# Kernel tuning notes

Measured on AMD Instinct MI355X. Metric: run time of the kernel, lower is better.

## Reference

```python
import jax, jax.numpy as jnp
import numpy as np


def setup_inputs() -> dict:
    key = jax.random.key(0)
    kq, kk, kv = jax.random.split(key, 3)
    n, d = 8192, 32
    return {
        "Q": jax.random.normal(kq, (n, d), dtype=jnp.float32),
        "K": jax.random.normal(kk, (n, d), dtype=jnp.float32),
        "V": jax.random.normal(kv, (n, d), dtype=jnp.float32),
    }


def reference(Q, K, V):
    # FlashAttention-2 tiling with online softmax is mathematically equivalent
    # to full (unscaled, unmasked) softmax attention: O = softmax(Q K^T) V.
    # Note: the original module applies NO 1/sqrt(d) scaling.
    S = jnp.einsum("qd,kd->qk", Q, K)           # [n, n]
    P = jax.nn.softmax(S, axis=-1)                # numerically stable softmax
    return jnp.einsum("qk,kd->qd", P, V)         # [n, d]
```

## Files before the change

### kernel.cpp

```cpp
#include <hip/hip_runtime.h>
#include <hip/hip_bf16.h>

typedef __bf16 bf16x8 __attribute__((ext_vector_type(8)));
typedef __bf16 bf16x4 __attribute__((ext_vector_type(4)));
typedef float  f32x4  __attribute__((ext_vector_type(4)));
typedef unsigned short u16;

static constexpr int N = 8192;
static constexpr int D = 32;
static constexpr float L2E = 1.44269504088896340736f;
static constexpr float MSHIFT = 32.0f;

__device__ __forceinline__ void gl_lds16(const u16* g, u16* l) {
  __builtin_amdgcn_global_load_lds(
      (const __attribute__((address_space(1))) unsigned int*)g,
      (__attribute__((address_space(3))) unsigned int*)l, 16, 0, 0);
}

__global__ __launch_bounds__(256) void prep_kernel(
    const float* __restrict__ Q, const float* __restrict__ K,
    const float* __restrict__ V, u16* __restrict__ Qb, u16* __restrict__ Kb,
    u16* __restrict__ Vt) {
  __shared__ float tile[64][33];
  const int b = blockIdx.x;
  auto pack = [](float x, float y) -> unsigned int {
    u16 ux = __builtin_bit_cast(u16, (__bf16)x);
    u16 uy = __builtin_bit_cast(u16, (__bf16)y);
    return (unsigned int)ux | ((unsigned int)uy << 16);
  };
  if (b < 256) {
    const int i = (b * 256 + threadIdx.x) * 4;
    const float4 q = *reinterpret_cast<const float4*>(Q + i);
    const float4 k = *reinterpret_cast<const float4*>(K + i);
    uint2 qo = { pack(q.x * L2E, q.y * L2E), pack(q.z * L2E, q.w * L2E) };
    uint2 ko = { pack(k.x, k.y), pack(k.z, k.w) };
    *reinterpret_cast<uint2*>(Qb + i) = qo;
    *reinterpret_cast<uint2*>(Kb + i) = ko;
  } else {
    const int r0 = (b - 256) * 64;
    const int row = threadIdx.x >> 2;
    const int c0 = (threadIdx.x & 3) * 8;
    const float4 x0 = *reinterpret_cast<const float4*>(V + (size_t)(r0 + row) * D + c0);
    const float4 x1 = *reinterpret_cast<const float4*>(V + (size_t)(r0 + row) * D + c0 + 4);
    tile[row][c0 + 0] = x0.x; tile[row][c0 + 1] = x0.y;
    tile[row][c0 + 2] = x0.z; tile[row][c0 + 3] = x0.w;
    tile[row][c0 + 4] = x1.x; tile[row][c0 + 5] = x1.y;
    tile[row][c0 + 6] = x1.z; tile[row][c0 + 7] = x1.w;
    __syncthreads();
    const int d = threadIdx.x >> 3;
    const int kc = (threadIdx.x & 7) * 8;
    uint4 o;
    o.x = pack(tile[kc + 0][d], tile[kc + 1][d]);
    o.y = pack(tile[kc + 2][d], tile[kc + 3][d]);
    o.z = pack(tile[kc + 4][d], tile[kc + 5][d]);
    o.w = pack(tile[kc + 6][d], tile[kc + 7][d]);
    *reinterpret_cast<uint4*>(Vt + (size_t)d * N + r0 + kc) = o;
  }
}

template <int NS>
__global__ __launch_bounds__(256, 4) void flash_kernel(
    const u16* __restrict__ Qb, const u16* __restrict__ Kb,
    const u16* __restrict__ Vt, float* __restrict__ lP,
    float* __restrict__ OP) {
  constexpr int KPB = N / NS;
  constexpr int NT = KPB / 64;
  __shared__ u16 Ks[2][2048];
  __shared__ u16 Vs[2][2048];

  const int tid = threadIdx.x;
  const int lane = tid & 63;
  const int wave = tid >> 6;
  const int a = lane & 15;
  const int g = lane >> 4;
  const int qg = blockIdx.x & 63;
  const int sp = blockIdx.x >> 6;
  const int qr0 = qg * 128 + wave * 32;
  const int k0 = sp * KPB;

  const bf16x8 qfA = *reinterpret_cast<const bf16x8*>(Qb + (qr0 + a) * D + g * 8);
  const bf16x8 qfB = *reinterpret_cast<const bf16x8*>(Qb + (qr0 + 16 + a) * D + g * 8);

  const int krow = tid >> 2;
  const int kslot = (tid & 3) ^ ((krow >> 1) & 3);
  const u16* __restrict__ ksrc = Kb + krow * D + kslot * 8;
  const int vd = tid >> 3;
  const int vlb = (tid & 7) ^ (vd & 7);
  const u16* __restrict__ vsrc = Vt + (size_t)vd * N + vlb * 8;
  u16* const kdst = &Ks[0][0] + wave * 512;
  u16* const vdst = &Vs[0][0] + wave * 512;

  const f32x4 minit = {-MSHIFT, -MSHIFT, -MSHIFT, -MSHIFT};
  const f32x4 zero4 = {0.f, 0.f, 0.f, 0.f};
  f32x4 accA0 = zero4, accA1 = zero4, accB0 = zero4, accB1 = zero4;
  float lA = 0.f, lB = 0.f;

  gl_lds16(ksrc + (size_t)k0 * D, kdst);
  gl_lds16(vsrc + k0, vdst);
  __syncthreads();

#pragma unroll
  for (int t = 0; t < NT; ++t) {
    const int cur = t & 1;
    if (t + 1 < NT) {
      const int kb = k0 + (t + 1) * 64;
      gl_lds16(ksrc + (size_t)kb * D, kdst + (cur ^ 1) * 2048);
      gl_lds16(vsrc + kb, vdst + (cur ^ 1) * 2048);
    }
    __builtin_amdgcn_sched_barrier(0);

    bf16x8 kf[4];
#pragma unroll
    for (int t4 = 0; t4 < 4; ++t4) {
      const int row = 16 * t4 + a;
      kf[t4] = *reinterpret_cast<const bf16x8*>(
          &Ks[cur][row * 32 + ((g ^ ((a >> 1) & 3)) << 3)]);
    }
    bf16x4 v0[4], v1[4];
#pragma unroll
    for (int tt = 0; tt < 4; ++tt) {
      const int pb = ((tt << 1) + (g >> 1)) ^ (a & 7);
      const int off = pb * 8 + (g & 1) * 4;
      v0[tt] = *reinterpret_cast<const bf16x4*>(&Vs[cur][a * 64 + off]);
      v1[tt] = *reinterpret_cast<const bf16x4*>(&Vs[cur][(16 + a) * 64 + off]);
    }

    f32x4 sA[4], sB[4];
#pragma unroll
    for (int t4 = 0; t4 < 4; ++t4) {
      sA[t4] = __builtin_amdgcn_mfma_f32_16x16x32_bf16(kf[t4], qfA, minit, 0, 0, 0);
      sB[t4] = __builtin_amdgcn_mfma_f32_16x16x32_bf16(kf[t4], qfB, minit, 0, 0, 0);
    }

    float pA[4][4], pB[4][4];
    float psA = 0.f, psB = 0.f;
#pragma unroll
    for (int t4 = 0; t4 < 4; ++t4) {
      float sa = 0.f, sb = 0.f;
#pragma unroll
      for (int r = 0; r < 4; ++r) {
        pA[t4][r] = __builtin_amdgcn_exp2f(sA[t4][r]);
        pB[t4][r] = __builtin_amdgcn_exp2f(sB[t4][r]);
        sa += pA[t4][r];
        sb += pB[t4][r];
      }
      psA += sa;
      psB += sb;
    }
    lA += psA;
    lB += psB;

    const bf16x8 pfA0 = {(__bf16)pA[0][0], (__bf16)pA[0][1], (__bf16)pA[0][2], (__bf16)pA[0][3],
                         (__bf16)pA[1][0], (__bf16)pA[1][1], (__bf16)pA[1][2], (__bf16)pA[1][3]};
    const bf16x8 pfA1 = {(__bf16)pA[2][0], (__bf16)pA[2][1], (__bf16)pA[2][2], (__bf16)pA[2][3],
                         (__bf16)pA[3][0], (__bf16)pA[3][1], (__bf16)pA[3][2], (__bf16)pA[3][3]};
    const bf16x8 pfB0 = {(__bf16)pB[0][0], (__bf16)pB[0][1], (__bf16)pB[0][2], (__bf16)pB[0][3],
                         (__bf16)pB[1][0], (__bf16)pB[1][1], (__bf16)pB[1][2], (__bf16)pB[1][3]};
    const bf16x8 pfB1 = {(__bf16)pB[2][0], (__bf16)pB[2][1], (__bf16)pB[2][2], (__bf16)pB[2][3],
                         (__bf16)pB[3][0], (__bf16)pB[3][1], (__bf16)pB[3][2], (__bf16)pB[3][3]};

    const bf16x8 va00 = __builtin_shufflevector(v0[0], v0[1], 0, 1, 2, 3, 4, 5, 6, 7);
    const bf16x8 va01 = __builtin_shufflevector(v0[2], v0[3], 0, 1, 2, 3, 4, 5, 6, 7);
    const bf16x8 va10 = __builtin_shufflevector(v1[0], v1[1], 0, 1, 2, 3, 4, 5, 6, 7);
    const bf16x8 va11 = __builtin_shufflevector(v1[2], v1[3], 0, 1, 2, 3, 4, 5, 6, 7);

    accA0 = __builtin_amdgcn_mfma_f32_16x16x32_bf16(va00, pfA0, accA0, 0, 0, 0);
    accA1 = __builtin_amdgcn_mfma_f32_16x16x32_bf16(va10, pfA0, accA1, 0, 0, 0);
    accB0 = __builtin_amdgcn_mfma_f32_16x16x32_bf16(va00, pfB0, accB0, 0, 0, 0);
    accB1 = __builtin_amdgcn_mfma_f32_16x16x32_bf16(va10, pfB0, accB1, 0, 0, 0);
    accA0 = __builtin_amdgcn_mfma_f32_16x16x32_bf16(va01, pfA1, accA0, 0, 0, 0);
    accA1 = __builtin_amdgcn_mfma_f32_16x16x32_bf16(va11, pfA1, accA1, 0, 0, 0);
    accB0 = __builtin_amdgcn_mfma_f32_16x16x32_bf16(va01, pfB1, accB0, 0, 0, 0);
    accB1 = __builtin_amdgcn_mfma_f32_16x16x32_bf16(va11, pfB1, accB1, 0, 0, 0);

    __syncthreads();
  }

  lA += __shfl_xor(lA, 16, 64);
  lA += __shfl_xor(lA, 32, 64);
  lB += __shfl_xor(lB, 16, 64);
  lB += __shfl_xor(lB, 32, 64);

  float* obA = OP + (size_t)(sp * N + qr0 + a) * D;
  float* obB = OP + (size_t)(sp * N + qr0 + 16 + a) * D;
#pragma unroll
  for (int r = 0; r < 4; ++r) {
    obA[4 * g + r] = accA0[r];
    obA[16 + 4 * g + r] = accA1[r];
    obB[4 * g + r] = accB0[r];
    obB[16 + 4 * g + r] = accB1[r];
  }
  if (g == 0) {
    lP[sp * N + qr0 + a] = lA;
    lP[sp * N + qr0 + 16 + a] = lB;
  }
}

template <int NS>
__global__ __launch_bounds__(256) void combine_kernel(
    const float* __restrict__ lP, const float* __restrict__ OP,
    float* __restrict__ out) {
  const int idx = blockIdx.x * 256 + threadIdx.x;
  if (idx >= N * D) return;
  const int q = idx >> 5;
  float L = 0.f, o = 0.f;
#pragma unroll
  for (int s = 0; s < NS; ++s) {
    L += lP[s * N + q];
    o += OP[(size_t)s * N * D + idx];
  }
  out[idx] = o / L;
}

extern "C" void kernel_launch(void* const* d_in, const int* in_sizes, int n_in,
                              void* d_out, int out_size, void* d_ws, size_t ws_size,
                              hipStream_t stream) {
  const float* Q = (const float*)d_in[0];
  const float* K = (const float*)d_in[1];
  const float* V = (const float*)d_in[2];
  float* out = (float*)d_out;

  const size_t base = (size_t)3 * N * D * sizeof(u16);
  const size_t per_split = (size_t)N * sizeof(float) + (size_t)N * D * sizeof(float);
  int ns = 16;
  while (ns > 4 && base + (size_t)ns * per_split > ws_size) ns >>= 1;

  u16* Qb = (u16*)d_ws;
  u16* Kb = Qb + N * D;
  u16* Vt = Kb + N * D;
  float* lP = (float*)(Vt + N * D);
  float* OP = lP + ns * N;

  prep_kernel<<<256 + N / 64, 256, 0, stream>>>(Q, K, V, Qb, Kb, Vt);
  switch (ns) {
    case 16:
      flash_kernel<16><<<64 * 16, 256, 0, stream>>>(Qb, Kb, Vt, lP, OP);
      combine_kernel<16><<<(N * D) / 256, 256, 0, stream>>>(lP, OP, out);
      break;
    case 8:
      flash_kernel<8><<<64 * 8, 256, 0, stream>>>(Qb, Kb, Vt, lP, OP);
      combine_kernel<8><<<(N * D) / 256, 256, 0, stream>>>(lP, OP, out);
      break;
    default:
      flash_kernel<4><<<64 * 4, 256, 0, stream>>>(Qb, Kb, Vt, lP, OP);
      combine_kernel<4><<<(N * D) / 256, 256, 0, stream>>>(lP, OP, out);
      break;
  }
}
```

Baseline: 33.91 us.

## Double key tile per iteration, add MFMA priority hints, vectorize partial-output stores and combine

The flash kernel now loads 128 keys per pipeline stage instead of 64, which halves the number of barriers and prefetch rounds. Each stage is processed as two 64-key halves with a new V swizzle for the 128-wide layout. It adds s_setprio around the MFMA groups and interleaves the A and B query halves so exp work can overlap with matrix ops. Partial-output stores and the combine kernel use float4 vectors, and the combine multiplies by a reciprocal instead of dividing. In exchange, LDS use doubles, which may reduce occupancy, and the fixed split count leaves fewer iterations to pipeline.

```diff
diff --git a/kernel.cpp b/kernel.cpp
--- a/kernel.cpp
+++ b/kernel.cpp
@@ -64,9 +64,9 @@
     const u16* __restrict__ Vt, float* __restrict__ lP,
     float* __restrict__ OP) {
   constexpr int KPB = N / NS;
-  constexpr int NT = KPB / 64;
-  __shared__ u16 Ks[2][2048];
-  __shared__ u16 Vs[2][2048];
+  constexpr int NT = KPB / 128;
+  __shared__ u16 Ks[2][4096];
+  __shared__ u16 Vs[2][4096];
 
   const int tid = threadIdx.x;
   const int lane = tid & 63;
@@ -84,9 +84,10 @@
   const int krow = tid >> 2;
   const int kslot = (tid & 3) ^ ((krow >> 1) & 3);
   const u16* __restrict__ ksrc = Kb + krow * D + kslot * 8;
-  const int vd = tid >> 3;
-  const int vlb = (tid & 7) ^ (vd & 7);
-  const u16* __restrict__ vsrc = Vt + (size_t)vd * N + vlb * 8;
+  const int vd = tid >> 4;
+  const int vblk = (tid & 15) ^ vd;
+  const u16* __restrict__ vsrcA = Vt + (size_t)vd * N + vblk * 8;
+  const u16* __restrict__ vsrcB = vsrcA + 16 * (size_t)N;
   u16* const kdst = &Ks[0][0] + wave * 512;
   u16* const vdst = &Vs[0][0] + wave * 512;
 
@@ -96,82 +97,114 @@
   float lA = 0.f, lB = 0.f;
 
   gl_lds16(ksrc + (size_t)k0 * D, kdst);
-  gl_lds16(vsrc + k0, vdst);
+  gl_lds16(ksrc + (size_t)(k0 + 64) * D, kdst + 2048);
+  gl_lds16(vsrcA + k0, vdst);
+  gl_lds16(vsrcB + k0, vdst + 2048);
   __syncthreads();
 
 #pragma unroll
   for (int t = 0; t < NT; ++t) {
     const int cur = t & 1;
     if (t + 1 < NT) {
-      const int kb = k0 + (t + 1) * 64;
-      gl_lds16(ksrc + (size_t)kb * D, kdst + (cur ^ 1) * 2048);
-      gl_lds16(vsrc + kb, vdst + (cur ^ 1) * 2048);
+      const int kb = k0 + (t + 1) * 128;
+      u16* kd = kdst + (cur ^ 1) * 4096;
+      u16* vd2 = vdst + (cur ^ 1) * 4096;
+      gl_lds16(ksrc + (size_t)kb * D, kd);
+      gl_lds16(ksrc + (size_t)(kb + 64) * D, kd + 2048);
+      gl_lds16(vsrcA + kb, vd2);
+      gl_lds16(vsrcB + kb, vd2 + 2048);
     }
     __builtin_amdgcn_sched_barrier(0);
 
-    bf16x8 kf[4];
-#pragma unroll
-    for (int t4 = 0; t4 < 4; ++t4) {
-      const int row = 16 * t4 + a;
-      kf[t4] = *reinterpret_cast<const bf16x8*>(
-          &Ks[cur][row * 32 + ((g ^ ((a >> 1) & 3)) << 3)]);
+#pragma unroll
+    for (int h = 0; h < 2; ++h) {
+      bf16x8 kf[4];
+#pragma unroll
+      for (int t4 = 0; t4 < 4; ++t4) {
+        const int row = 64 * h + 16 * t4 + a;
+        kf[t4] = *reinterpret_cast<const bf16x8*>(
+            &Ks[cur][row * 32 + ((g ^ ((a >> 1) & 3)) << 3)]);
+      }
+
+      bf16x8 pfA0, pfA1, pfB0, pfB1;
+      float psA = 0.f, psB = 0.f;
+      {
+        f32x4 s[4];
+        __builtin_amdgcn_s_setprio(1);
+#pragma unroll
+        for (int t4 = 0; t4 < 4; ++t4)
+          s[t4] = __builtin_amdgcn_mfma_f32_16x16x32_bf16(kf[t4], qfA, minit, 0, 0, 0);
+        __builtin_amdgcn_s_setprio(0);
+        float p[4][4];
+#pragma unroll
+        for (int t4 = 0; t4 < 4; ++t4)
+#pragma unroll
+          for (int r = 0; r < 4; ++r) {
+            p[t4][r] = __builtin_amdgcn_exp2f(s[t4][r]);
+            psA += p[t4][r];
+          }
+        pfA0 = bf16x8{(__bf16)p[0][0], (__bf16)p[0][1], (__bf16)p[0][2], (__bf16)p[0][3],
+                      (__bf16)p[1][0], (__bf16)p[1][1], (__bf16)p[1][2], (__bf16)p[1][3]};
+        pfA1 = bf16x8{(__bf16)p[2][0], (__bf16)p[2][1], (__bf16)p[2][2], (__bf16)p[2][3],
+                      (__bf16)p[3][0], (__bf16)p[3][1], (__bf16)p[3][2], (__bf16)p[3][3]};
+      }
+      {
+        f32x4 s[4];
+        __builtin_amdgcn_s_setprio(1);
+#pragma unroll
+        for (int t4 = 0; t4 < 4; ++t4)
+          s[t4] = __builtin_amdgcn_mfma_f32_16x16x32_bf16(kf[t4], qfB, minit, 0, 0, 0);
+        __builtin_amdgcn_s_setprio(0);
+        float p[4][4];
+#pragma unroll
+        for (int t4 = 0; t4 < 4; ++t4)
+#pragma unroll
+          for (int r = 0; r < 4; ++r) {
+            p[t4][r] = __builtin_amdgcn_exp2f(s[t4][r]);
+            psB += p[t4][r];
+          }
+        pfB0 = bf16x8{(__bf16)p[0][0], (__bf16)p[0][1], (__bf16)p[0][2], (__bf16)p[0][3],
+                      (__bf16)p[1][0], (__bf16)p[1][1], (__bf16)p[1][2], (__bf16)p[1][3]};
+        pfB1 = bf16x8{(__bf16)p[2][0], (__bf16)p[2][1], (__bf16)p[2][2], (__bf16)p[2][3],
+                      (__bf16)p[3][0], (__bf16)p[3][1], (__bf16)p[3][2], (__bf16)p[3][3]};
+      }
+      lA += psA;
+      lB += psB;
+
+      bf16x8 va00, va01, va10, va11;
+      {
+        const int u0 = 2 * h, u1 = 2 * h + 1;
+        const int e0 = (g & 1) * 4;
+        const int lb00 = 4 * u0 + (g >> 1), lb01 = lb00 + 2;
+        const int lb10 = 4 * u1 + (g >> 1), lb11 = lb10 + 2;
+        const u16* r0 = &Vs[cur][a * 128];
+        const u16* r1 = &Vs[cur][(16 + a) * 128];
+        const int x = a;
+        const bf16x4 p00 = *reinterpret_cast<const bf16x4*>(r0 + (lb00 ^ x) * 8 + e0);
+        const bf16x4 p01 = *reinterpret_cast<const bf16x4*>(r0 + (lb01 ^ x) * 8 + e0);
+        const bf16x4 p02 = *reinterpret_cast<const bf16x4*>(r0 + (lb10 ^ x) * 8 + e0);
+        const bf16x4 p03 = *reinterpret_cast<const bf16x4*>(r0 + (lb11 ^ x) * 8 + e0);
+        const bf16x4 p10 = *reinterpret_cast<const bf16x4*>(r1 + (lb00 ^ x) * 8 + e0);
+        const bf16x4 p11 = *reinterpret_cast<const bf16x4*>(r1 + (lb01 ^ x) * 8 + e0);
+        const bf16x4 p12 = *reinterpret_cast<const bf16x4*>(r1 + (lb10 ^ x) * 8 + e0);
+        const bf16x4 p13 = *reinterpret_cast<const bf16x4*>(r1 + (lb11 ^ x) * 8 + e0);
+        va00 = __builtin_shufflevector(p00, p01, 0, 1, 2, 3, 4, 5, 6, 7);
+        va01 = __builtin_shufflevector(p02, p03, 0, 1, 2, 3, 4, 5, 6, 7);
+        va10 = __builtin_shufflevector(p10, p11, 0, 1, 2, 3, 4, 5, 6, 7);
+        va11 = __builtin_shufflevector(p12, p13, 0, 1, 2, 3, 4, 5, 6, 7);
+      }
+
+      __builtin_amdgcn_s_setprio(1);
+      accA0 = __builtin_amdgcn_mfma_f32_16x16x32_bf16(va00, pfA0, accA0, 0, 0, 0);
+      accA1 = __builtin_amdgcn_mfma_f32_16x16x32_bf16(va10, pfA0, accA1, 0, 0, 0);
+      accB0 = __builtin_amdgcn_mfma_f32_16x16x32_bf16(va00, pfB0, accB0, 0, 0, 0);
+      accB1 = __builtin_amdgcn_mfma_f32_16x16x32_bf16(va10, pfB0, accB1, 0, 0, 0);
+      accA0 = __builtin_amdgcn_mfma_f32_16x16x32_bf16(va01, pfA1, accA0, 0, 0, 0);
+      accA1 = __builtin_amdgcn_mfma_f32_16x16x32_bf16(va11, pfA1, accA1, 0, 0, 0);
+      accB0 = __builtin_amdgcn_mfma_f32_16x16x32_bf16(va01, pfB1, accB0, 0, 0, 0);
+      accB1 = __builtin_amdgcn_mfma_f32_16x16x32_bf16(va11, pfB1, accB1, 0, 0, 0);
+      __builtin_amdgcn_s_setprio(0);
     }
-    bf16x4 v0[4], v1[4];
-#pragma unroll
-    for (int tt = 0; tt < 4; ++tt) {
-      const int pb = ((tt << 1) + (g >> 1)) ^ (a & 7);
-      const int off = pb * 8 + (g & 1) * 4;
-      v0[tt] = *reinterpret_cast<const bf16x4*>(&Vs[cur][a * 64 + off]);
-      v1[tt] = *reinterpret_cast<const bf16x4*>(&Vs[cur][(16 + a) * 64 + off]);
-    }
-
-    f32x4 sA[4], sB[4];
-#pragma unroll
-    for (int t4 = 0; t4 < 4; ++t4) {
-      sA[t4] = __builtin_amdgcn_mfma_f32_16x16x32_bf16(kf[t4], qfA, minit, 0, 0, 0);
-      sB[t4] = __builtin_amdgcn_mfma_f32_16x16x32_bf16(kf[t4], qfB, minit, 0, 0, 0);
-    }
-
-    float pA[4][4], pB[4][4];
-    float psA = 0.f, psB = 0.f;
-#pragma unroll
-    for (int t4 = 0; t4 < 4; ++t4) {
-      float sa = 0.f, sb = 0.f;
-#pragma unroll
-      for (int r = 0; r < 4; ++r) {
-        pA[t4][r] = __builtin_amdgcn_exp2f(sA[t4][r]);
-        pB[t4][r] = __builtin_amdgcn_exp2f(sB[t4][r]);
-        sa += pA[t4][r];
-        sb += pB[t4][r];
-      }
-      psA += sa;
-      psB += sb;
-    }
-    lA += psA;
-    lB += psB;
-
-    const bf16x8 pfA0 = {(__bf16)pA[0][0], (__bf16)pA[0][1], (__bf16)pA[0][2], (__bf16)pA[0][3],
-                         (__bf16)pA[1][0], (__bf16)pA[1][1], (__bf16)pA[1][2], (__bf16)pA[1][3]};
-    const bf16x8 pfA1 = {(__bf16)pA[2][0], (__bf16)pA[2][1], (__bf16)pA[2][2], (__bf16)pA[2][3],
-                         (__bf16)pA[3][0], (__bf16)pA[3][1], (__bf16)pA[3][2], (__bf16)pA[3][3]};
-    const bf16x8 pfB0 = {(__bf16)pB[0][0], (__bf16)pB[0][1], (__bf16)pB[0][2], (__bf16)pB[0][3],
-                         (__bf16)pB[1][0], (__bf16)pB[1][1], (__bf16)pB[1][2], (__bf16)pB[1][3]};
-    const bf16x8 pfB1 = {(__bf16)pB[2][0], (__bf16)pB[2][1], (__bf16)pB[2][2], (__bf16)pB[2][3],
-                         (__bf16)pB[3][0], (__bf16)pB[3][1], (__bf16)pB[3][2], (__bf16)pB[3][3]};
-
-    const bf16x8 va00 = __builtin_shufflevector(v0[0], v0[1], 0, 1, 2, 3, 4, 5, 6, 7);
-    const bf16x8 va01 = __builtin_shufflevector(v0[2], v0[3], 0, 1, 2, 3, 4, 5, 6, 7);
-    const bf16x8 va10 = __builtin_shufflevector(v1[0], v1[1], 0, 1, 2, 3, 4, 5, 6, 7);
-    const bf16x8 va11 = __builtin_shufflevector(v1[2], v1[3], 0, 1, 2, 3, 4, 5, 6, 7);
-
-    accA0 = __builtin_amdgcn_mfma_f32_16x16x32_bf16(va00, pfA0, accA0, 0, 0, 0);
-    accA1 = __builtin_amdgcn_mfma_f32_16x16x32_bf16(va10, pfA0, accA1, 0, 0, 0);
-    accB0 = __builtin_amdgcn_mfma_f32_16x16x32_bf16(va00, pfB0, accB0, 0, 0, 0);
-    accB1 = __builtin_amdgcn_mfma_f32_16x16x32_bf16(va10, pfB0, accB1, 0, 0, 0);
-    accA0 = __builtin_amdgcn_mfma_f32_16x16x32_bf16(va01, pfA1, accA0, 0, 0, 0);
-    accA1 = __builtin_amdgcn_mfma_f32_16x16x32_bf16(va11, pfA1, accA1, 0, 0, 0);
-    accB0 = __builtin_amdgcn_mfma_f32_16x16x32_bf16(va01, pfB1, accB0, 0, 0, 0);
-    accB1 = __builtin_amdgcn_mfma_f32_16x16x32_bf16(va11, pfB1, accB1, 0, 0, 0);
 
     __syncthreads();
   }
@@ -183,13 +216,10 @@
 
   float* obA = OP + (size_t)(sp * N + qr0 + a) * D;
   float* obB = OP + (size_t)(sp * N + qr0 + 16 + a) * D;
-#pragma unroll
-  for (int r = 0; r < 4; ++r) {
-    obA[4 * g + r] = accA0[r];
-    obA[16 + 4 * g + r] = accA1[r];
-    obB[4 * g + r] = accB0[r];
-    obB[16 + 4 * g + r] = accB1[r];
-  }
+  *reinterpret_cast<f32x4*>(obA + 4 * g) = accA0;
+  *reinterpret_cast<f32x4*>(obA + 16 + 4 * g) = accA1;
+  *reinterpret_cast<f32x4*>(obB + 4 * g) = accB0;
+  *reinterpret_cast<f32x4*>(obB + 16 + 4 * g) = accB1;
   if (g == 0) {
     lP[sp * N + qr0 + a] = lA;
     lP[sp * N + qr0 + 16 + a] = lB;
@@ -200,16 +230,18 @@
 __global__ __launch_bounds__(256) void combine_kernel(
     const float* __restrict__ lP, const float* __restrict__ OP,
     float* __restrict__ out) {
-  const int idx = blockIdx.x * 256 + threadIdx.x;
-  if (idx >= N * D) return;
-  const int q = idx >> 5;
-  float L = 0.f, o = 0.f;
+  const int idx4 = blockIdx.x * 256 + threadIdx.x;
+  if (idx4 >= (N * D) / 4) return;
+  const int q = idx4 >> 3;
+  float L = 0.f;
+  f32x4 o = {0.f, 0.f, 0.f, 0.f};
 #pragma unroll
   for (int s = 0; s < NS; ++s) {
     L += lP[s * N + q];
-    o += OP[(size_t)s * N * D + idx];
-  }
-  out[idx] = o / L;
+    o += *reinterpret_cast<const f32x4*>(OP + (size_t)s * N * D + (size_t)idx4 * 4);
+  }
+  const float inv = 1.0f / L;
+  *reinterpret_cast<f32x4*>(out + (size_t)idx4 * 4) = o * inv;
 }
 
 extern "C" void kernel_launch(void* const* d_in, const int* in_sizes, int n_in,
@@ -235,15 +267,15 @@
   switch (ns) {
     case 16:
       flash_kernel<16><<<64 * 16, 256, 0, stream>>>(Qb, Kb, Vt, lP, OP);
-      combine_kernel<16><<<(N * D) / 256, 256, 0, stream>>>(lP, OP, out);
+      combine_kernel<16><<<(N * D) / 1024, 256, 0, stream>>>(lP, OP, out);
       break;
     case 8:
       flash_kernel<8><<<64 * 8, 256, 0, stream>>>(Qb, Kb, Vt, lP, OP);
-      combine_kernel<8><<<(N * D) / 256, 256, 0, stream>>>(lP, OP, out);
+      combine_kernel<8><<<(N * D) / 1024, 256, 0, stream>>>(lP, OP, out);
       break;
     default:
       flash_kernel<4><<<64 * 4, 256, 0, stream>>>(Qb, Kb, Vt, lP, OP);
-      combine_kernel<4><<<(N * D) / 256, 256, 0, stream>>>(lP, OP, out);
+      combine_kernel<4><<<(N * D) / 1024, 256, 0, stream>>>(lP, OP, out);
       break;
   }
 }
```

After: 35.44 us. 4.5% more time.

## Fuse split-K combine into flash kernel and give each wave private staging buffers

Applied to the files above, without the earlier changes.

Removes the separate combine kernel. Each flash block now bumps an atomic counter per query group, and the last-arriving block reduces the partial outputs for that group. The counters are reset in the prep kernel. Each wave now loads its own K/V tile into private LDS buffers and waits with waitcnt instead of a block-wide __syncthreads per tile. The split count drops from 16 to 8, which cuts parallelism, occupancy is lowered to 2, and the output stores are vectorised. The atomic tail serializes some work on the last block, and each wave now fetches the full K/V tile redundantly.

```diff
diff --git a/kernel.cpp b/kernel.cpp
--- a/kernel.cpp
+++ b/kernel.cpp
@@ -20,9 +20,10 @@
 __global__ __launch_bounds__(256) void prep_kernel(
     const float* __restrict__ Q, const float* __restrict__ K,
     const float* __restrict__ V, u16* __restrict__ Qb, u16* __restrict__ Kb,
-    u16* __restrict__ Vt) {
+    u16* __restrict__ Vt, int* __restrict__ cnt) {
   __shared__ float tile[64][33];
   const int b = blockIdx.x;
+  if (b == 0 && threadIdx.x < 64) cnt[threadIdx.x] = 0;
   auto pack = [](float x, float y) -> unsigned int {
     u16 ux = __builtin_bit_cast(u16, (__bf16)x);
     u16 uy = __builtin_bit_cast(u16, (__bf16)y);
@@ -59,71 +60,76 @@
 }
 
 template <int NS>
-__global__ __launch_bounds__(256, 4) void flash_kernel(
+__global__ __launch_bounds__(256, 2) void flash_kernel(
     const u16* __restrict__ Qb, const u16* __restrict__ Kb,
     const u16* __restrict__ Vt, float* __restrict__ lP,
-    float* __restrict__ OP) {
+    float* __restrict__ OP, float* __restrict__ out, int* __restrict__ cnt) {
   constexpr int KPB = N / NS;
   constexpr int NT = KPB / 64;
-  __shared__ u16 Ks[2][2048];
-  __shared__ u16 Vs[2][2048];
+  __shared__ u16 Ks[4][2][2048];
+  __shared__ u16 Vs[4][2][2048];
+  __shared__ int last_flag;
 
   const int tid = threadIdx.x;
   const int lane = tid & 63;
-  const int wave = tid >> 6;
+  const int w = tid >> 6;
   const int a = lane & 15;
   const int g = lane >> 4;
   const int qg = blockIdx.x & 63;
   const int sp = blockIdx.x >> 6;
-  const int qr0 = qg * 128 + wave * 32;
+  const int qr0 = qg * 128 + w * 32;
   const int k0 = sp * KPB;
 
   const bf16x8 qfA = *reinterpret_cast<const bf16x8*>(Qb + (qr0 + a) * D + g * 8);
   const bf16x8 qfB = *reinterpret_cast<const bf16x8*>(Qb + (qr0 + 16 + a) * D + g * 8);
 
-  const int krow = tid >> 2;
-  const int kslot = (tid & 3) ^ ((krow >> 1) & 3);
-  const u16* __restrict__ ksrc = Kb + krow * D + kslot * 8;
-  const int vd = tid >> 3;
-  const int vlb = (tid & 7) ^ (vd & 7);
-  const u16* __restrict__ vsrc = Vt + (size_t)vd * N + vlb * 8;
-  u16* const kdst = &Ks[0][0] + wave * 512;
-  u16* const vdst = &Vs[0][0] + wave * 512;
+  const int kslot = (lane & 3) ^ ((lane >> 3) & 3);
+  const u16* __restrict__ kS = Kb + (lane >> 2) * D + kslot * 8;
+  const int vblk = (lane & 7) ^ ((lane >> 3) & 7);
+  const u16* __restrict__ vS = Vt + (size_t)(lane >> 3) * N + vblk * 8;
 
   const f32x4 minit = {-MSHIFT, -MSHIFT, -MSHIFT, -MSHIFT};
   const f32x4 zero4 = {0.f, 0.f, 0.f, 0.f};
   f32x4 accA0 = zero4, accA1 = zero4, accB0 = zero4, accB1 = zero4;
   float lA = 0.f, lB = 0.f;
 
-  gl_lds16(ksrc + (size_t)k0 * D, kdst);
-  gl_lds16(vsrc + k0, vdst);
-  __syncthreads();
-
-#pragma unroll
+  auto STAGE = [&](int buf, int kb) {
+    u16* kd = &Ks[w][buf][0];
+    u16* vd = &Vs[w][buf][0];
+#pragma unroll
+    for (int i = 0; i < 4; ++i)
+      gl_lds16(kS + (size_t)(kb + 16 * i) * D, kd + i * 512);
+#pragma unroll
+    for (int j = 0; j < 4; ++j)
+      gl_lds16(vS + kb + (size_t)j * 8 * N, vd + j * 512);
+  };
+
+  STAGE(0, k0);
+  __builtin_amdgcn_s_waitcnt(0x0F70);
+  __builtin_amdgcn_sched_barrier(0);
+
+#pragma unroll 2
   for (int t = 0; t < NT; ++t) {
     const int cur = t & 1;
-    if (t + 1 < NT) {
-      const int kb = k0 + (t + 1) * 64;
-      gl_lds16(ksrc + (size_t)kb * D, kdst + (cur ^ 1) * 2048);
-      gl_lds16(vsrc + kb, vdst + (cur ^ 1) * 2048);
-    }
+    bf16x8 kf[4];
+#pragma unroll
+    for (int t4 = 0; t4 < 4; ++t4)
+      kf[t4] = *reinterpret_cast<const bf16x8*>(
+          &Ks[w][cur][(16 * t4 + a) * 32 + ((g ^ ((a >> 1) & 3)) << 3)]);
+    const int pa = a & 7, e0 = (g & 1) * 4, gh = g >> 1;
+    auto vld = [&](int drow, int u) -> bf16x8 {
+      const int lb0 = 4 * u + gh, lb1 = lb0 + 2;
+      const bf16x4 x0 = *reinterpret_cast<const bf16x4*>(
+          &Vs[w][cur][drow * 64 + ((lb0 ^ pa) << 3) + e0]);
+      const bf16x4 x1 = *reinterpret_cast<const bf16x4*>(
+          &Vs[w][cur][drow * 64 + ((lb1 ^ pa) << 3) + e0]);
+      return __builtin_shufflevector(x0, x1, 0, 1, 2, 3, 4, 5, 6, 7);
+    };
+    const bf16x8 va00 = vld(a, 0), va01 = vld(a, 1);
+    const bf16x8 va10 = vld(16 + a, 0), va11 = vld(16 + a, 1);
+
+    if (t + 1 < NT) STAGE(cur ^ 1, k0 + (t + 1) * 64);
     __builtin_amdgcn_sched_barrier(0);
-
-    bf16x8 kf[4];
-#pragma unroll
-    for (int t4 = 0; t4 < 4; ++t4) {
-      const int row = 16 * t4 + a;
-      kf[t4] = *reinterpret_cast<const bf16x8*>(
-          &Ks[cur][row * 32 + ((g ^ ((a >> 1) & 3)) << 3)]);
-    }
-    bf16x4 v0[4], v1[4];
-#pragma unroll
-    for (int tt = 0; tt < 4; ++tt) {
-      const int pb = ((tt << 1) + (g >> 1)) ^ (a & 7);
-      const int off = pb * 8 + (g & 1) * 4;
-      v0[tt] = *reinterpret_cast<const bf16x4*>(&Vs[cur][a * 64 + off]);
-      v1[tt] = *reinterpret_cast<const bf16x4*>(&Vs[cur][(16 + a) * 64 + off]);
-    }
 
     f32x4 sA[4], sB[4];
 #pragma unroll
@@ -131,22 +137,22 @@
       sA[t4] = __builtin_amdgcn_mfma_f32_16x16x32_bf16(kf[t4], qfA, minit, 0, 0, 0);
       sB[t4] = __builtin_amdgcn_mfma_f32_16x16x32_bf16(kf[t4], qfB, minit, 0, 0, 0);
     }
-
     float pA[4][4], pB[4][4];
-    float psA = 0.f, psB = 0.f;
-#pragma unroll
-    for (int t4 = 0; t4 < 4; ++t4) {
-      float sa = 0.f, sb = 0.f;
+#pragma unroll
+    for (int t4 = 0; t4 < 4; ++t4)
 #pragma unroll
       for (int r = 0; r < 4; ++r) {
         pA[t4][r] = __builtin_amdgcn_exp2f(sA[t4][r]);
         pB[t4][r] = __builtin_amdgcn_exp2f(sB[t4][r]);
-        sa += pA[t4][r];
-        sb += pB[t4][r];
       }
-      psA += sa;
-      psB += sb;
-    }
+    float psA = 0.f, psB = 0.f;
+#pragma unroll
+    for (int t4 = 0; t4 < 4; ++t4)
+#pragma unroll
+      for (int r = 0; r < 4; ++r) {
+        psA += pA[t4][r];
+        psB += pB[t4][r];
+      }
     lA += psA;
     lB += psB;
 
@@ -159,11 +165,6 @@
     const bf16x8 pfB1 = {(__bf16)pB[2][0], (__bf16)pB[2][1], (__bf16)pB[2][2], (__bf16)pB[2][3],
                          (__bf16)pB[3][0], (__bf16)pB[3][1], (__bf16)pB[3][2], (__bf16)pB[3][3]};
 
-    const bf16x8 va00 = __builtin_shufflevector(v0[0], v0[1], 0, 1, 2, 3, 4, 5, 6, 7);
-    const bf16x8 va01 = __builtin_shufflevector(v0[2], v0[3], 0, 1, 2, 3, 4, 5, 6, 7);
-    const bf16x8 va10 = __builtin_shufflevector(v1[0], v1[1], 0, 1, 2, 3, 4, 5, 6, 7);
-    const bf16x8 va11 = __builtin_shufflevector(v1[2], v1[3], 0, 1, 2, 3, 4, 5, 6, 7);
-
     accA0 = __builtin_amdgcn_mfma_f32_16x16x32_bf16(va00, pfA0, accA0, 0, 0, 0);
     accA1 = __builtin_amdgcn_mfma_f32_16x16x32_bf16(va10, pfA0, accA1, 0, 0, 0);
     accB0 = __builtin_amdgcn_mfma_f32_16x16x32_bf16(va00, pfB0, accB0, 0, 0, 0);
@@ -173,7 +174,10 @@
     accB0 = __builtin_amdgcn_mfma_f32_16x16x32_bf16(va01, pfB1, accB0, 0, 0, 0);
     accB1 = __builtin_amdgcn_mfma_f32_16x16x32_bf16(va11, pfB1, accB1, 0, 0, 0);
 
-    __syncthreads();
+    if (t + 1 < NT) {
+      __builtin_amdgcn_s_waitcnt(0x0F70);
+      __builtin_amdgcn_sched_barrier(0);
+    }
   }
 
   lA += __shfl_xor(lA, 16, 64);
@@ -183,33 +187,41 @@
 
   float* obA = OP + (size_t)(sp * N + qr0 + a) * D;
   float* obB = OP + (size_t)(sp * N + qr0 + 16 + a) * D;
-#pragma unroll
-  for (int r = 0; r < 4; ++r) {
-    obA[4 * g + r] = accA0[r];
-    obA[16 + 4 * g + r] = accA1[r];
-    obB[4 * g + r] = accB0[r];
-    obB[16 + 4 * g + r] = accB1[r];
-  }
+  *reinterpret_cast<f32x4*>(obA + 4 * g) = accA0;
+  *reinterpret_cast<f32x4*>(obA + 16 + 4 * g) = accA1;
+  *reinterpret_cast<f32x4*>(obB + 4 * g) = accB0;
+  *reinterpret_cast<f32x4*>(obB + 16 + 4 * g) = accB1;
   if (g == 0) {
     lP[sp * N + qr0 + a] = lA;
     lP[sp * N + qr0 + 16 + a] = lB;
   }
-}
-
-template <int NS>
-__global__ __launch_bounds__(256) void combine_kernel(
-    const float* __restrict__ lP, const float* __restrict__ OP,
-    float* __restrict__ out) {
-  const int idx = blockIdx.x * 256 + threadIdx.x;
-  if (idx >= N * D) return;
-  const int q = idx >> 5;
-  float L = 0.f, o = 0.f;
-#pragma unroll
-  for (int s = 0; s < NS; ++s) {
-    L += lP[s * N + q];
-    o += OP[(size_t)s * N * D + idx];
-  }
-  out[idx] = o / L;
+
+  __syncthreads();
+  if (tid == 0) {
+    __threadfence();
+    const int v = __hip_atomic_fetch_add(&cnt[qg], 1, __ATOMIC_ACQ_REL,
+                                         __HIP_MEMORY_SCOPE_AGENT);
+    last_flag = (v == NS - 1);
+  }
+  __syncthreads();
+  if (last_flag) {
+    __threadfence();
+#pragma unroll
+    for (int k = 0; k < 4; ++k) {
+      const int i4 = k * 256 + tid;
+      const int q = qg * 128 + (i4 >> 3);
+      const int db = i4 & 7;
+      float L = 0.f;
+      f32x4 o = {0.f, 0.f, 0.f, 0.f};
+#pragma unroll
+      for (int s = 0; s < NS; ++s) {
+        L += lP[s * N + q];
+        o += *reinterpret_cast<const f32x4*>(OP + ((size_t)s * N + q) * D + db * 4);
+      }
+      const float inv = 1.0f / L;
+      *reinterpret_cast<f32x4*>(out + (size_t)q * D + db * 4) = o * inv;
+    }
+  }
 }
 
 extern "C" void kernel_launch(void* const* d_in, const int* in_sizes, int n_in,
@@ -222,28 +234,19 @@
 
   const size_t base = (size_t)3 * N * D * sizeof(u16);
   const size_t per_split = (size_t)N * sizeof(float) + (size_t)N * D * sizeof(float);
-  int ns = 16;
-  while (ns > 4 && base + (size_t)ns * per_split > ws_size) ns >>= 1;
+  int ns = 8;
+  while (ns > 4 && base + (size_t)ns * per_split + 256 > ws_size) ns >>= 1;
 
   u16* Qb = (u16*)d_ws;
   u16* Kb = Qb + N * D;
   u16* Vt = Kb + N * D;
   float* lP = (float*)(Vt + N * D);
   float* OP = lP + ns * N;
-
-  prep_kernel<<<256 + N / 64, 256, 0, stream>>>(Q, K, V, Qb, Kb, Vt);
-  switch (ns) {
-    case 16:
-      flash_kernel<16><<<64 * 16, 256, 0, stream>>>(Qb, Kb, Vt, lP, OP);
-      combine_kernel<16><<<(N * D) / 256, 256, 0, stream>>>(lP, OP, out);
-      break;
-    case 8:
-      flash_kernel<8><<<64 * 8, 256, 0, stream>>>(Qb, Kb, Vt, lP, OP);
-      combine_kernel<8><<<(N * D) / 256, 256, 0, stream>>>(lP, OP, out);
-      break;
-    default:
-      flash_kernel<4><<<64 * 4, 256, 0, stream>>>(Qb, Kb, Vt, lP, OP);
-      combine_kernel<4><<<(N * D) / 256, 256, 0, stream>>>(lP, OP, out);
-      break;
-  }
-}
+  int* cnt = (int*)(OP + (size_t)ns * N * D);
+
+  prep_kernel<<<256 + N / 64, 256, 0, stream>>>(Q, K, V, Qb, Kb, Vt, cnt);
+  if (ns == 8)
+    flash_kernel<8><<<64 * 8, 256, 0, stream>>>(Qb, Kb, Vt, lP, OP, out, cnt);
+  else
+    flash_kernel<4><<<64 * 4, 256, 0, stream>>>(Qb, Kb, Vt, lP, OP, out, cnt);
+}
```

Measured after the change: 52.53 us. 1.55x slower.

## Double query rows per wave to reuse K/V tiles, vectorize combine

Applied to the files above, without the earlier changes.

Each wave now handles 64 query rows instead of 32, so every K/V tile staged in LDS is reused across twice as many queries. The block count halves to 512 and launch bounds drop to 2 blocks per SIMD to leave room for the extra accumulators. Output stores and the combine kernel are vectorized to float4. The trade-off is fewer blocks on 256 CUs and higher register pressure, which lowers occupancy and leaves less latency to hide.

```diff
diff --git a/kernel.cpp b/kernel.cpp
--- a/kernel.cpp
+++ b/kernel.cpp
@@ -59,7 +59,7 @@
 }
 
 template <int NS>
-__global__ __launch_bounds__(256, 4) void flash_kernel(
+__global__ __launch_bounds__(256, 2) void flash_kernel(
     const u16* __restrict__ Qb, const u16* __restrict__ Kb,
     const u16* __restrict__ Vt, float* __restrict__ lP,
     float* __restrict__ OP) {
@@ -73,13 +73,15 @@
   const int wave = tid >> 6;
   const int a = lane & 15;
   const int g = lane >> 4;
-  const int qg = blockIdx.x & 63;
-  const int sp = blockIdx.x >> 6;
-  const int qr0 = qg * 128 + wave * 32;
+  const int qg = blockIdx.x & 31;
+  const int sp = blockIdx.x >> 5;
+  const int qr0 = qg * 256 + wave * 64;
   const int k0 = sp * KPB;
 
-  const bf16x8 qfA = *reinterpret_cast<const bf16x8*>(Qb + (qr0 + a) * D + g * 8);
-  const bf16x8 qfB = *reinterpret_cast<const bf16x8*>(Qb + (qr0 + 16 + a) * D + g * 8);
+  bf16x8 qf[4];
+#pragma unroll
+  for (int i = 0; i < 4; ++i)
+    qf[i] = *reinterpret_cast<const bf16x8*>(Qb + (qr0 + 16 * i + a) * D + g * 8);
 
   const int krow = tid >> 2;
   const int kslot = (tid & 3) ^ ((krow >> 1) & 3);
@@ -92,8 +94,10 @@
 
   const f32x4 minit = {-MSHIFT, -MSHIFT, -MSHIFT, -MSHIFT};
   const f32x4 zero4 = {0.f, 0.f, 0.f, 0.f};
-  f32x4 accA0 = zero4, accA1 = zero4, accB0 = zero4, accB1 = zero4;
-  float lA = 0.f, lB = 0.f;
+  f32x4 acc[4][2];
+#pragma unroll
+  for (int i = 0; i < 4; ++i) { acc[i][0] = zero4; acc[i][1] = zero4; }
+  float lsum[4] = {0.f, 0.f, 0.f, 0.f};
 
   gl_lds16(ksrc + (size_t)k0 * D, kdst);
   gl_lds16(vsrc + k0, vdst);
@@ -124,75 +128,56 @@
       v0[tt] = *reinterpret_cast<const bf16x4*>(&Vs[cur][a * 64 + off]);
       v1[tt] = *reinterpret_cast<const bf16x4*>(&Vs[cur][(16 + a) * 64 + off]);
     }
-
-    f32x4 sA[4], sB[4];
-#pragma unroll
-    for (int t4 = 0; t4 < 4; ++t4) {
-      sA[t4] = __builtin_amdgcn_mfma_f32_16x16x32_bf16(kf[t4], qfA, minit, 0, 0, 0);
-      sB[t4] = __builtin_amdgcn_mfma_f32_16x16x32_bf16(kf[t4], qfB, minit, 0, 0, 0);
-    }
-
-    float pA[4][4], pB[4][4];
-    float psA = 0.f, psB = 0.f;
-#pragma unroll
-    for (int t4 = 0; t4 < 4; ++t4) {
-      float sa = 0.f, sb = 0.f;
-#pragma unroll
-      for (int r = 0; r < 4; ++r) {
-        pA[t4][r] = __builtin_amdgcn_exp2f(sA[t4][r]);
-        pB[t4][r] = __builtin_amdgcn_exp2f(sB[t4][r]);
-        sa += pA[t4][r];
-        sb += pB[t4][r];
-      }
-      psA += sa;
-      psB += sb;
-    }
-    lA += psA;
-    lB += psB;
-
-    const bf16x8 pfA0 = {(__bf16)pA[0][0], (__bf16)pA[0][1], (__bf16)pA[0][2], (__bf16)pA[0][3],
-                         (__bf16)pA[1][0], (__bf16)pA[1][1], (__bf16)pA[1][2], (__bf16)pA[1][3]};
-    const bf16x8 pfA1 = {(__bf16)pA[2][0], (__bf16)pA[2][1], (__bf16)pA[2][2], (__bf16)pA[2][3],
-                         (__bf16)pA[3][0], (__bf16)pA[3][1], (__bf16)pA[3][2], (__bf16)pA[3][3]};
-    const bf16x8 pfB0 = {(__bf16)pB[0][0], (__bf16)pB[0][1], (__bf16)pB[0][2], (__bf16)pB[0][3],
-                         (__bf16)pB[1][0], (__bf16)pB[1][1], (__bf16)pB[1][2], (__bf16)pB[1][3]};
-    const bf16x8 pfB1 = {(__bf16)pB[2][0], (__bf16)pB[2][1], (__bf16)pB[2][2], (__bf16)pB[2][3],
-                         (__bf16)pB[3][0], (__bf16)pB[3][1], (__bf16)pB[3][2], (__bf16)pB[3][3]};
-
     const bf16x8 va00 = __builtin_shufflevector(v0[0], v0[1], 0, 1, 2, 3, 4, 5, 6, 7);
     const bf16x8 va01 = __builtin_shufflevector(v0[2], v0[3], 0, 1, 2, 3, 4, 5, 6, 7);
     const bf16x8 va10 = __builtin_shufflevector(v1[0], v1[1], 0, 1, 2, 3, 4, 5, 6, 7);
     const bf16x8 va11 = __builtin_shufflevector(v1[2], v1[3], 0, 1, 2, 3, 4, 5, 6, 7);
 
-    accA0 = __builtin_amdgcn_mfma_f32_16x16x32_bf16(va00, pfA0, accA0, 0, 0, 0);
-    accA1 = __builtin_amdgcn_mfma_f32_16x16x32_bf16(va10, pfA0, accA1, 0, 0, 0);
-    accB0 = __builtin_amdgcn_mfma_f32_16x16x32_bf16(va00, pfB0, accB0, 0, 0, 0);
-    accB1 = __builtin_amdgcn_mfma_f32_16x16x32_bf16(va10, pfB0, accB1, 0, 0, 0);
-    accA0 = __builtin_amdgcn_mfma_f32_16x16x32_bf16(va01, pfA1, accA0, 0, 0, 0);
-    accA1 = __builtin_amdgcn_mfma_f32_16x16x32_bf16(va11, pfA1, accA1, 0, 0, 0);
-    accB0 = __builtin_amdgcn_mfma_f32_16x16x32_bf16(va01, pfB1, accB0, 0, 0, 0);
-    accB1 = __builtin_amdgcn_mfma_f32_16x16x32_bf16(va11, pfB1, accB1, 0, 0, 0);
+#pragma unroll
+    for (int i = 0; i < 4; ++i) {
+      f32x4 s0 = __builtin_amdgcn_mfma_f32_16x16x32_bf16(kf[0], qf[i], minit, 0, 0, 0);
+      f32x4 s1 = __builtin_amdgcn_mfma_f32_16x16x32_bf16(kf[1], qf[i], minit, 0, 0, 0);
+      f32x4 s2 = __builtin_amdgcn_mfma_f32_16x16x32_bf16(kf[2], qf[i], minit, 0, 0, 0);
+      f32x4 s3 = __builtin_amdgcn_mfma_f32_16x16x32_bf16(kf[3], qf[i], minit, 0, 0, 0);
+      float p[16];
+#pragma unroll
+      for (int r = 0; r < 4; ++r) {
+        p[r]      = __builtin_amdgcn_exp2f(s0[r]);
+        p[4 + r]  = __builtin_amdgcn_exp2f(s1[r]);
+        p[8 + r]  = __builtin_amdgcn_exp2f(s2[r]);
+        p[12 + r] = __builtin_amdgcn_exp2f(s3[r]);
+      }
+      float ps = 0.f;
+#pragma unroll
+      for (int t4 = 0; t4 < 4; ++t4) {
+        float sa = 0.f;
+#pragma unroll
+        for (int r = 0; r < 4; ++r) sa += p[4 * t4 + r];
+        ps += sa;
+      }
+      lsum[i] += ps;
+      const bf16x8 pf0 = {(__bf16)p[0], (__bf16)p[1], (__bf16)p[2], (__bf16)p[3],
+                          (__bf16)p[4], (__bf16)p[5], (__bf16)p[6], (__bf16)p[7]};
+      const bf16x8 pf1 = {(__bf16)p[8], (__bf16)p[9], (__bf16)p[10], (__bf16)p[11],
+                          (__bf16)p[12], (__bf16)p[13], (__bf16)p[14], (__bf16)p[15]};
+      acc[i][0] = __builtin_amdgcn_mfma_f32_16x16x32_bf16(va00, pf0, acc[i][0], 0, 0, 0);
+      acc[i][1] = __builtin_amdgcn_mfma_f32_16x16x32_bf16(va10, pf0, acc[i][1], 0, 0, 0);
+      acc[i][0] = __builtin_amdgcn_mfma_f32_16x16x32_bf16(va01, pf1, acc[i][0], 0, 0, 0);
+      acc[i][1] = __builtin_amdgcn_mfma_f32_16x16x32_bf16(va11, pf1, acc[i][1], 0, 0, 0);
+    }
 
     __syncthreads();
   }
 
-  lA += __shfl_xor(lA, 16, 64);
-  lA += __shfl_xor(lA, 32, 64);
-  lB += __shfl_xor(lB, 16, 64);
-  lB += __shfl_xor(lB, 32, 64);
-
-  float* obA = OP + (size_t)(sp * N + qr0 + a) * D;
-  float* obB = OP + (size_t)(sp * N + qr0 + 16 + a) * D;
-#pragma unroll
-  for (int r = 0; r < 4; ++r) {
-    obA[4 * g + r] = accA0[r];
-    obA[16 + 4 * g + r] = accA1[r];
-    obB[4 * g + r] = accB0[r];
-    obB[16 + 4 * g + r] = accB1[r];
-  }
-  if (g == 0) {
-    lP[sp * N + qr0 + a] = lA;
-    lP[sp * N + qr0 + 16 + a] = lB;
+#pragma unroll
+  for (int i = 0; i < 4; ++i) {
+    float l = lsum[i];
+    l += __shfl_xor(l, 16, 64);
+    l += __shfl_xor(l, 32, 64);
+    float* ob = OP + (size_t)(sp * N + qr0 + 16 * i + a) * D;
+    *reinterpret_cast<f32x4*>(ob + 4 * g) = acc[i][0];
+    *reinterpret_cast<f32x4*>(ob + 16 + 4 * g) = acc[i][1];
+    if (g == 0) lP[sp * N + qr0 + 16 * i + a] = l;
   }
 }
 
@@ -200,16 +185,18 @@
 __global__ __launch_bounds__(256) void combine_kernel(
     const float* __restrict__ lP, const float* __restrict__ OP,
     float* __restrict__ out) {
-  const int idx = blockIdx.x * 256 + threadIdx.x;
-  if (idx >= N * D) return;
-  const int q = idx >> 5;
-  float L = 0.f, o = 0.f;
+  const int idx4 = blockIdx.x * 256 + threadIdx.x;
+  if (idx4 >= (N * D) / 4) return;
+  const int q = idx4 >> 3;
+  float L = 0.f;
+  f32x4 o = {0.f, 0.f, 0.f, 0.f};
 #pragma unroll
   for (int s = 0; s < NS; ++s) {
     L += lP[s * N + q];
-    o += OP[(size_t)s * N * D + idx];
-  }
-  out[idx] = o / L;
+    o += *reinterpret_cast<const f32x4*>(OP + (size_t)s * N * D + (size_t)idx4 * 4);
+  }
+  const float inv = 1.0f / L;
+  *reinterpret_cast<f32x4*>(out + (size_t)idx4 * 4) = o * inv;
 }
 
 extern "C" void kernel_launch(void* const* d_in, const int* in_sizes, int n_in,
@@ -234,16 +221,16 @@
   prep_kernel<<<256 + N / 64, 256, 0, stream>>>(Q, K, V, Qb, Kb, Vt);
   switch (ns) {
     case 16:
-      flash_kernel<16><<<64 * 16, 256, 0, stream>>>(Qb, Kb, Vt, lP, OP);
-      combine_kernel<16><<<(N * D) / 256, 256, 0, stream>>>(lP, OP, out);
+      flash_kernel<16><<<32 * 16, 256, 0, stream>>>(Qb, Kb, Vt, lP, OP);
+      combine_kernel<16><<<(N * D) / 1024, 256, 0, stream>>>(lP, OP, out);
       break;
     case 8:
-      flash_kernel<8><<<64 * 8, 256, 0, stream>>>(Qb, Kb, Vt, lP, OP);
-      combine_kernel<8><<<(N * D) / 256, 256, 0, stream>>>(lP, OP, out);
+      flash_kernel<8><<<32 * 8, 256, 0, stream>>>(Qb, Kb, Vt, lP, OP);
+      combine_kernel<8><<<(N * D) / 1024, 256, 0, stream>>>(lP, OP, out);
       break;
     default:
-      flash_kernel<4><<<64 * 4, 256, 0, stream>>>(Qb, Kb, Vt, lP, OP);
-      combine_kernel<4><<<(N * D) / 256, 256, 0, stream>>>(lP, OP, out);
+      flash_kernel<4><<<32 * 4, 256, 0, stream>>>(Qb, Kb, Vt, lP, OP);
+      combine_kernel<4><<<(N * D) / 1024, 256, 0, stream>>>(lP, OP, out);
       break;
   }
 }
```

Result: slower. 81.91 us (+141.6%).
